# Optimization experiments

Measured on AMD Instinct MI355X. Metric: run time of the kernel, lower is better.

The kernel has to match this reference:

```python
import jax, jax.numpy as jnp
import numpy as np

TOTAL = 262144
NUM_SEG = 1024
H_DIM = 64
BF = 2  # block_flag_num
EPS = 1e-5


def setup_inputs() -> dict:
    key = jax.random.key(0)
    ks = jax.random.split(key, 12)
    # equal-length contiguous segments (ragged in general; equal here for setup)
    bounds = np.arange(0, TOTAL + 1, TOTAL // NUM_SEG, dtype=np.int64)
    seq_start_end = jnp.asarray(np.stack([bounds[:-1], bounds[1:]], axis=1))
    d_in = BF * 2          # 4
    d_emb = BF * 16        # 32
    d_pre = d_emb + H_DIM  # 96
    s = lambda n: 1.0 / np.sqrt(n)
    return {
        'h_state': jax.random.normal(ks[0], (TOTAL, H_DIM), jnp.float32),
        'end_block_pos_rel': jax.random.normal(ks[1], (TOTAL, 2, BF), jnp.float32),
        'W_sp': jax.random.normal(ks[2], (d_emb, d_in), jnp.float32) * s(d_in),
        'b_sp': jnp.zeros((d_emb,), jnp.float32),
        'W1': jax.random.normal(ks[3], (512, d_pre), jnp.float32) * s(d_pre),
        'b1': jnp.zeros((512,), jnp.float32),
        'g1': jnp.ones((512,), jnp.float32),
        'be1': jnp.zeros((512,), jnp.float32),
        'W2': jax.random.normal(ks[4], (1024, 512), jnp.float32) * s(512),
        'b2': jnp.zeros((1024,), jnp.float32),
        'g2': jnp.ones((1024,), jnp.float32),
        'be2': jnp.zeros((1024,), jnp.float32),
        'seq_start_end': seq_start_end,
    }


def _segment_bn(x, seg_ids, counts, gamma, beta):
    # training-mode BatchNorm1d computed independently per segment (biased var)
    num_seg = counts.shape[0]
    mean = jax.ops.segment_sum(x, seg_ids, num_segments=num_seg) / counts[:, None]
    ex2 = jax.ops.segment_sum(x * x, seg_ids, num_segments=num_seg) / counts[:, None]
    var = ex2 - mean * mean
    xn = (x - mean[seg_ids]) * jax.lax.rsqrt(var[seg_ids] + EPS)
    return xn * gamma + beta


def reference(h_state, end_block_pos_rel, W_sp, b_sp, W1, b1, g1, be1, W2, b2, g2, be2, seq_start_end):
    total = h_state.shape[0]
    starts = seq_start_end[:, 0]
    # contiguous segments: segment id of each row
    seg_ids = jnp.searchsorted(starts, jnp.arange(total), side='right') - 1
    counts = (seq_start_end[:, 1] - seq_start_end[:, 0]).astype(h_state.dtype)
    # permute(0,2,1).view(n,-1): (total, 2, BF) -> (total, BF*2)
    pos = jnp.transpose(end_block_pos_rel, (0, 2, 1)).reshape(total, -1)
    rel_emb = pos @ W_sp.T + b_sp                              # (total, 32)
    mlp_in = jnp.concatenate([rel_emb, h_state], axis=1)       # (total, 96)
    h1 = jax.nn.relu(_segment_bn(mlp_in @ W1.T + b1, seg_ids, counts, g1, be1))
    out = jax.nn.relu(_segment_bn(h1 @ W2.T + b2, seg_ids, counts, g2, be2))
    return out  # (total, 1024)
```

## Files before the change

kernel.cpp:

```cpp
#include <hip/hip_runtime.h>
#include <hip/hip_bf16.h>

#define TOTALROWS 262144
#define NSEG      1024
#define SEGROWS   256
#define HD        64
#define DEMB      32
#define DPRE      96
#define N1        512
#define N2        1024
#define EPSB      1e-5f

typedef short s16x8 __attribute__((ext_vector_type(8)));
typedef float f32x4 __attribute__((ext_vector_type(4)));

static __device__ __forceinline__ ushort f2bf(float x) {
    union { float f; unsigned u; } v; v.f = x;
    unsigned r = v.u + 0x7FFFu + ((v.u >> 16) & 1u);
    return (ushort)(r >> 16);
}

static __device__ __forceinline__ void gload_lds16(const void* g, void* l) {
    __builtin_amdgcn_global_load_lds(
        (const __attribute__((address_space(1))) void*)g,
        (__attribute__((address_space(3))) void*)l, 16, 0, 0);
}

__global__ void convert_w2_kernel(const float* __restrict__ w2, ushort* __restrict__ w2b) {
    int i = blockIdx.x * 256 + threadIdx.x;
    float4 v = ((const float4*)w2)[i];
    ushort4 o;
    o.x = f2bf(v.x); o.y = f2bf(v.y); o.z = f2bf(v.z); o.w = f2bf(v.w);
    ((ushort4*)w2b)[i] = o;
}

__global__ __launch_bounds__(512, 2) void layer1_kernel(
    const float* __restrict__ hstate, const float* __restrict__ ebpr,
    const float* __restrict__ Wsp, const float* __restrict__ W1,
    const float* __restrict__ g1, const float* __restrict__ be1,
    ushort* __restrict__ h1)
{
    __shared__ __align__(16) ushort As[SEGROWS * 104];
    __shared__ __align__(16) ushort Bs[SEGROWS * 104];
    __shared__ float statsS[8][4][16];
    __shared__ float statsQ[8][4][16];

    const int seg  = blockIdx.x;
    const int ct   = blockIdx.y;
    const int tid  = threadIdx.x;
    const int lane = tid & 63, wid = tid >> 6;
    const int wr   = wid >> 2, wc = wid & 3;

    {
        const float4* hs4 = (const float4*)(hstate + (size_t)seg * SEGROWS * HD);
        #pragma unroll
        for (int i = 0; i < 8; ++i) {
            int u = tid + i * 512;
            int r = u >> 4, c4 = u & 15;
            float4 v = hs4[u];
            ushort* dst = &As[r * 104 + DEMB + c4 * 4];
            dst[0] = f2bf(v.x); dst[1] = f2bf(v.y); dst[2] = f2bf(v.z); dst[3] = f2bf(v.w);
        }
        #pragma unroll
        for (int i = 0; i < 16; ++i) {
            int u = tid + i * 512;
            int r = u >> 5, k = u & 31;
            float4 e = ((const float4*)ebpr)[seg * SEGROWS + r];
            float4 w = ((const float4*)Wsp)[k];
            float val = w.x * e.x + w.y * e.z + w.z * e.y + w.w * e.w;
            As[r * 104 + k] = f2bf(val);
        }
    }
    {
        const float4* w14 = (const float4*)(W1 + (size_t)ct * 256 * DPRE);
        #pragma unroll
        for (int i = 0; i < 12; ++i) {
            int u = tid + i * 512;
            int r = u / 24, c4 = u % 24;
            float4 v = w14[u];
            ushort* dst = &Bs[r * 104 + c4 * 4];
            dst[0] = f2bf(v.x); dst[1] = f2bf(v.y); dst[2] = f2bf(v.z); dst[3] = f2bf(v.w);
        }
    }
    __syncthreads();

    f32x4 acc[8][4] = {};
    const int arow0 = wr * 128 + (lane & 15);
    const int bcol0 = wc * 64  + (lane & 15);
    const int kg    = (lane >> 4) * 8;
    #pragma unroll
    for (int ks = 0; ks < 3; ++ks) {
        s16x8 af[8], bfr[4];
        #pragma unroll
        for (int m = 0; m < 8; ++m)
            af[m] = *(const s16x8*)&As[(arow0 + m * 16) * 104 + ks * 32 + kg];
        #pragma unroll
        for (int n = 0; n < 4; ++n)
            bfr[n] = *(const s16x8*)&Bs[(bcol0 + n * 16) * 104 + ks * 32 + kg];
        #pragma unroll
        for (int m = 0; m < 8; ++m)
            #pragma unroll
            for (int n = 0; n < 4; ++n)
                acc[m][n] = __builtin_amdgcn_mfma_f32_16x16x32_bf16(af[m], bfr[n], acc[m][n], 0, 0, 0);
    }

    float s[4], q[4];
    #pragma unroll
    for (int n = 0; n < 4; ++n) { s[n] = 0.f; q[n] = 0.f; }
    #pragma unroll
    for (int m = 0; m < 8; ++m)
        #pragma unroll
        for (int n = 0; n < 4; ++n)
            #pragma unroll
            for (int j = 0; j < 4; ++j) { float v = acc[m][n][j]; s[n] += v; q[n] += v * v; }
    #pragma unroll
    for (int n = 0; n < 4; ++n) {
        s[n] += __shfl_xor(s[n], 16); q[n] += __shfl_xor(q[n], 16);
        s[n] += __shfl_xor(s[n], 32); q[n] += __shfl_xor(q[n], 32);
    }
    if ((lane >> 4) == 0) {
        #pragma unroll
        for (int n = 0; n < 4; ++n) { statsS[wid][n][lane] = s[n]; statsQ[wid][n][lane] = q[n]; }
    }
    __syncthreads();

    const float inv256 = 1.0f / 256.0f;
    float aa[4], bb[4];
    const int c16 = lane & 15;
    #pragma unroll
    for (int n = 0; n < 4; ++n) {
        float sum = statsS[wc][n][c16] + statsS[4 + wc][n][c16];
        float sq  = statsQ[wc][n][c16] + statsQ[4 + wc][n][c16];
        float mean = sum * inv256;
        float var  = sq * inv256 - mean * mean;
        float rinv = rsqrtf(var + EPSB);
        int col = ct * 256 + wc * 64 + n * 16 + c16;
        aa[n] = g1[col] * rinv;
        bb[n] = be1[col] - mean * aa[n];
    }

    ushort* outp = h1 + (size_t)(seg * SEGROWS) * N1 + ct * 256;
    const int rbase = wr * 128 + (lane >> 4) * 4;
    #pragma unroll
    for (int m = 0; m < 8; ++m)
        #pragma unroll
        for (int j = 0; j < 4; ++j) {
            int r = rbase + m * 16 + j;
            ushort* rowp = outp + (size_t)r * N1 + wc * 64 + c16;
            #pragma unroll
            for (int n = 0; n < 4; ++n) {
                float v = acc[m][n][j] * aa[n] + bb[n];
                v = v > 0.f ? v : 0.f;
                rowp[n * 16] = f2bf(v);
            }
        }
}


static __device__ __forceinline__ void stage_step(
    const char* gA, const char* gB, ushort* lA, ushort* lB,
    int t, int wid, int lane)
{
    const int rsub = lane >> 2;
    const int cb   = (((lane & 3) ^ ((lane >> 3) & 3)) << 4);
    #pragma unroll
    for (int i = 0; i < 2; ++i) {
        int g = i * 8 + wid;
        size_t go = (size_t)(g * 16 + rsub) * 1024 + (size_t)t * 64 + cb;
        gload_lds16(gA + go, (char*)lA + g * 1024);
        gload_lds16(gB + go, (char*)lB + g * 1024);
    }
}

static __device__ __forceinline__ void compute_step(
    const ushort* lA, const ushort* lB, f32x4 (&acc)[8][4],
    int arow0, int bcol0, int swz)
{
    s16x8 af[8], bfr[4];
    #pragma unroll
    for (int m = 0; m < 8; ++m)
        af[m] = *(const s16x8*)&lA[(arow0 + m * 16) * 32 + swz];
    #pragma unroll
    for (int n = 0; n < 4; ++n)
        bfr[n] = *(const s16x8*)&lB[(bcol0 + n * 16) * 32 + swz];
    __builtin_amdgcn_s_setprio(1);
    #pragma unroll
    for (int m = 0; m < 8; ++m)
        #pragma unroll
        for (int n = 0; n < 4; ++n)
            acc[m][n] = __builtin_amdgcn_mfma_f32_16x16x32_bf16(af[m], bfr[n], acc[m][n], 0, 0, 0);
    __builtin_amdgcn_s_setprio(0);
}

__global__ __launch_bounds__(512, 2) void layer2_kernel(
    const ushort* __restrict__ h1, const ushort* __restrict__ W2b,
    const float* __restrict__ g2, const float* __restrict__ be2,
    float* __restrict__ out)
{
    __shared__ __align__(16) ushort As[4][SEGROWS * 32];
    __shared__ __align__(16) ushort Bs[4][256 * 32];
    __shared__ float statsS[8][4][16];
    __shared__ float statsQ[8][4][16];

    const int b   = blockIdx.x;
    const int wg  = (b & 7) * 512 + (b >> 3);
    const int seg = wg >> 2;
    const int ct  = wg & 3;

    const int tid  = threadIdx.x;
    const int lane = tid & 63, wid = tid >> 6;
    const int wr   = wid >> 2, wc = wid & 3;

    const char* srcA = (const char*)(h1  + (size_t)seg * SEGROWS * N1);
    const char* srcB = (const char*)(W2b + (size_t)ct  * 256    * N1);

    f32x4 acc[8][4] = {};
    const int arow0 = wr * 128 + (lane & 15);
    const int bcol0 = wc * 64  + (lane & 15);
    const int swz  = (((lane >> 4) ^ ((lane >> 1) & 3)) << 3);

    stage_step(srcA, srcB, As[0], Bs[0], 0, wid, lane);
    stage_step(srcA, srcB, As[1], Bs[1], 1, wid, lane);
    stage_step(srcA, srcB, As[2], Bs[2], 2, wid, lane);

#define L2_STEP(T, VW)                                                           \
    {                                                                            \
        if ((T) + 3 < 16)                                                        \
            stage_step(srcA, srcB, As[((T)+3)&3], Bs[((T)+3)&3], (T)+3, wid, lane); \
        asm volatile("s_waitcnt vmcnt(" #VW ")" ::: "memory");                   \
        __builtin_amdgcn_s_barrier();                                            \
        compute_step(As[(T)&3], Bs[(T)&3], acc, arow0, bcol0, swz);              \
        __builtin_amdgcn_s_barrier();                                            \
    }

    L2_STEP(0, 12)  L2_STEP(1, 12)  L2_STEP(2, 12)  L2_STEP(3, 12)
    L2_STEP(4, 12)  L2_STEP(5, 12)  L2_STEP(6, 12)  L2_STEP(7, 12)
    L2_STEP(8, 12)  L2_STEP(9, 12)  L2_STEP(10, 12) L2_STEP(11, 12)
    L2_STEP(12, 12) L2_STEP(13, 8)  L2_STEP(14, 4)  L2_STEP(15, 0)
#undef L2_STEP

    float s[4], q[4];
    #pragma unroll
    for (int n = 0; n < 4; ++n) { s[n] = 0.f; q[n] = 0.f; }
    #pragma unroll
    for (int m = 0; m < 8; ++m)
        #pragma unroll
        for (int n = 0; n < 4; ++n)
            #pragma unroll
            for (int j = 0; j < 4; ++j) { float v = acc[m][n][j]; s[n] += v; q[n] += v * v; }
    #pragma unroll
    for (int n = 0; n < 4; ++n) {
        s[n] += __shfl_xor(s[n], 16); q[n] += __shfl_xor(q[n], 16);
        s[n] += __shfl_xor(s[n], 32); q[n] += __shfl_xor(q[n], 32);
    }
    if ((lane >> 4) == 0) {
        #pragma unroll
        for (int n = 0; n < 4; ++n) { statsS[wid][n][lane] = s[n]; statsQ[wid][n][lane] = q[n]; }
    }
    __syncthreads();

    const float inv256 = 1.0f / 256.0f;
    float aa[4], bb[4];
    const int c16 = lane & 15;
    #pragma unroll
    for (int n = 0; n < 4; ++n) {
        float sum = statsS[wc][n][c16] + statsS[4 + wc][n][c16];
        float sq  = statsQ[wc][n][c16] + statsQ[4 + wc][n][c16];
        float mean = sum * inv256;
        float var  = sq * inv256 - mean * mean;
        float rinv = rsqrtf(var + EPSB);
        int col = ct * 256 + wc * 64 + n * 16 + c16;
        aa[n] = g2[col] * rinv;
        bb[n] = be2[col] - mean * aa[n];
    }

    float* outp = out + (size_t)(seg * SEGROWS) * N2 + ct * 256;
    const int rbase = wr * 128 + (lane >> 4) * 4;
    #pragma unroll
    for (int m = 0; m < 8; ++m)
        #pragma unroll
        for (int j = 0; j < 4; ++j) {
            int r = rbase + m * 16 + j;
            float* rowp = outp + (size_t)r * N2 + wc * 64 + c16;
            #pragma unroll
            for (int n = 0; n < 4; ++n) {
                float v = acc[m][n][j] * aa[n] + bb[n];
                v = v > 0.f ? v : 0.f;
                rowp[n * 16] = v;
            }
        }
}

extern "C" void kernel_launch(void* const* d_in, const int* in_sizes, int n_in,
                              void* d_out, int out_size, void* d_ws, size_t ws_size,
                              hipStream_t stream) {
    const float* hstate = (const float*)d_in[0];
    const float* ebpr   = (const float*)d_in[1];
    const float* Wsp    = (const float*)d_in[2];
    const float* W1     = (const float*)d_in[4];
    const float* g1     = (const float*)d_in[6];
    const float* be1    = (const float*)d_in[7];
    const float* W2     = (const float*)d_in[8];
    const float* g2     = (const float*)d_in[10];
    const float* be2    = (const float*)d_in[11];
    float* outp         = (float*)d_out;

    ushort* h1  = (ushort*)d_ws;
    ushort* W2b = h1 + (size_t)TOTALROWS * N1;

    convert_w2_kernel<<<dim3((N2 * N1 / 4) / 256), dim3(256), 0, stream>>>(W2, W2b);
    layer1_kernel<<<dim3(NSEG, 2), dim3(512), 0, stream>>>(hstate, ebpr, Wsp, W1, g1, be1, h1);
    layer2_kernel<<<dim3(4096), dim3(512), 0, stream>>>(h1, W2b, g2, be2, outp);
}
```

Measured before the change: 634.8 us.

## Restructure layer2 GEMM main loop into four-phase ping-pong with interleaved staging

The layer2 GEMM main loop now uses K tiles of 64 instead of 32, with double-buffered LDS split into row halves and a new XOR swizzle. Each K tile runs as four MFMA quadrant phases, and each phase issues part of the next tile's global-to-LDS loads between the fragment reads and its barrier. The aim is to hide load latency behind MFMA work and to halve the number of loop iterations and barrier pairs. In exchange it adds more barriers per tile, keeps more fragments live in registers, and adds intricate buffer-reuse ordering that could race if the waitcnt and barrier placement is wrong.

```diff
diff --git a/kernel.cpp b/kernel.cpp
--- a/kernel.cpp
+++ b/kernel.cpp
@@ -157,48 +157,64 @@
 }
 
 
-static __device__ __forceinline__ void stage_step(
-    const char* gA, const char* gB, ushort* lA, ushort* lB,
-    int t, int wid, int lane)
-{
-    const int rsub = lane >> 2;
-    const int cb   = (((lane & 3) ^ ((lane >> 3) & 3)) << 4);
-    #pragma unroll
-    for (int i = 0; i < 2; ++i) {
-        int g = i * 8 + wid;
-        size_t go = (size_t)(g * 16 + rsub) * 1024 + (size_t)t * 64 + cb;
-        gload_lds16(gA + go, (char*)lA + g * 1024);
-        gload_lds16(gB + go, (char*)lB + g * 1024);
-    }
-}
-
-static __device__ __forceinline__ void compute_step(
-    const ushort* lA, const ushort* lB, f32x4 (&acc)[8][4],
-    int arow0, int bcol0, int swz)
-{
-    s16x8 af[8], bfr[4];
-    #pragma unroll
-    for (int m = 0; m < 8; ++m)
-        af[m] = *(const s16x8*)&lA[(arow0 + m * 16) * 32 + swz];
-    #pragma unroll
-    for (int n = 0; n < 4; ++n)
-        bfr[n] = *(const s16x8*)&lB[(bcol0 + n * 16) * 32 + swz];
+static __device__ __forceinline__ void stage_half(
+    const char* gsrc, char* ldst, int kt, int wid, int lane)
+{
+    const int row = (wid << 3) + (lane >> 3);
+    const int cl  = (lane & 7) ^ (lane >> 3);
+    const char* g = gsrc + (size_t)row * 1024 + (size_t)kt * 128 + cl * 16;
+    gload_lds16(g,          ldst + wid * 1024);
+    gload_lds16(g + 65536,  ldst + 8192 + wid * 1024);
+}
+
+static __device__ __forceinline__ void read_a4(
+    s16x8 (&dst)[4][2], const ushort* base, int arow0, int mofs, int ko0, int ko1)
+{
+    #pragma unroll
+    for (int mi = 0; mi < 4; ++mi) {
+        const ushort* p = base + (arow0 + (mofs + mi) * 16) * 64;
+        dst[mi][0] = *(const s16x8*)(p + ko0);
+        dst[mi][1] = *(const s16x8*)(p + ko1);
+    }
+}
+static __device__ __forceinline__ void read_b2(
+    s16x8 (&dst)[2][2], const ushort* base, int bcol0, int nofs, int ko0, int ko1)
+{
+    #pragma unroll
+    for (int ni = 0; ni < 2; ++ni) {
+        const ushort* p = base + (bcol0 + (nofs + ni) * 16) * 64;
+        dst[ni][0] = *(const s16x8*)(p + ko0);
+        dst[ni][1] = *(const s16x8*)(p + ko1);
+    }
+}
+static __device__ __forceinline__ void mfma_q(
+    f32x4 (&acc)[8][4], const s16x8 (&af)[4][2], const s16x8 (&bfr)[2][2],
+    int mofs, int nofs)
+{
     __builtin_amdgcn_s_setprio(1);
     #pragma unroll
-    for (int m = 0; m < 8; ++m)
-        #pragma unroll
-        for (int n = 0; n < 4; ++n)
-            acc[m][n] = __builtin_amdgcn_mfma_f32_16x16x32_bf16(af[m], bfr[n], acc[m][n], 0, 0, 0);
+    for (int mi = 0; mi < 4; ++mi)
+        #pragma unroll
+        for (int ni = 0; ni < 2; ++ni) {
+            f32x4 c = acc[mofs + mi][nofs + ni];
+            c = __builtin_amdgcn_mfma_f32_16x16x32_bf16(af[mi][0], bfr[ni][0], c, 0, 0, 0);
+            c = __builtin_amdgcn_mfma_f32_16x16x32_bf16(af[mi][1], bfr[ni][1], c, 0, 0, 0);
+            acc[mofs + mi][nofs + ni] = c;
+        }
     __builtin_amdgcn_s_setprio(0);
 }
+
+#define PHASE_BAR() do { __builtin_amdgcn_sched_barrier(0); \
+    asm volatile("s_barrier" ::: "memory"); \
+    __builtin_amdgcn_sched_barrier(0); } while (0)
 
 __global__ __launch_bounds__(512, 2) void layer2_kernel(
     const ushort* __restrict__ h1, const ushort* __restrict__ W2b,
     const float* __restrict__ g2, const float* __restrict__ be2,
     float* __restrict__ out)
 {
-    __shared__ __align__(16) ushort As[4][SEGROWS * 32];
-    __shared__ __align__(16) ushort Bs[4][256 * 32];
+    __shared__ __align__(16) ushort Asl[2 * 256 * 64];
+    __shared__ __align__(16) ushort Bsl[2 * 256 * 64];
     __shared__ float statsS[8][4][16];
     __shared__ float statsQ[8][4][16];
 
@@ -217,27 +233,52 @@
     f32x4 acc[8][4] = {};
     const int arow0 = wr * 128 + (lane & 15);
     const int bcol0 = wc * 64  + (lane & 15);
-    const int swz  = (((lane >> 4) ^ ((lane >> 1) & 3)) << 3);
-
-    stage_step(srcA, srcB, As[0], Bs[0], 0, wid, lane);
-    stage_step(srcA, srcB, As[1], Bs[1], 1, wid, lane);
-    stage_step(srcA, srcB, As[2], Bs[2], 2, wid, lane);
-
-#define L2_STEP(T, VW)                                                           \
-    {                                                                            \
-        if ((T) + 3 < 16)                                                        \
-            stage_step(srcA, srcB, As[((T)+3)&3], Bs[((T)+3)&3], (T)+3, wid, lane); \
-        asm volatile("s_waitcnt vmcnt(" #VW ")" ::: "memory");                   \
-        __builtin_amdgcn_s_barrier();                                            \
-        compute_step(As[(T)&3], Bs[(T)&3], acc, arow0, bcol0, swz);              \
-        __builtin_amdgcn_s_barrier();                                            \
-    }
-
-    L2_STEP(0, 12)  L2_STEP(1, 12)  L2_STEP(2, 12)  L2_STEP(3, 12)
-    L2_STEP(4, 12)  L2_STEP(5, 12)  L2_STEP(6, 12)  L2_STEP(7, 12)
-    L2_STEP(8, 12)  L2_STEP(9, 12)  L2_STEP(10, 12) L2_STEP(11, 12)
-    L2_STEP(12, 12) L2_STEP(13, 8)  L2_STEP(14, 4)  L2_STEP(15, 0)
-#undef L2_STEP
+    const int ko0 = (((lane >> 4)    ) ^ (lane & 7)) * 8;
+    const int ko1 = (((lane >> 4) + 4) ^ (lane & 7)) * 8;
+
+    stage_half(srcA,          (char*)Asl,          0, wid, lane);
+    stage_half(srcA + 131072, (char*)Asl + 16384,  0, wid, lane);
+    stage_half(srcB,          (char*)Bsl,          0, wid, lane);
+    stage_half(srcB + 131072, (char*)Bsl + 16384,  0, wid, lane);
+    stage_half(srcA,          (char*)Asl + 32768,  1, wid, lane);
+    asm volatile("s_waitcnt vmcnt(2)" ::: "memory");
+    PHASE_BAR();
+
+#define L2_TILE(U, VW)                                                              \
+    {                                                                               \
+        const ushort* Ab = Asl + ((U) & 1) * 16384;                                 \
+        const ushort* Bb = Bsl + ((U) & 1) * 16384;                                 \
+        char* Acur = (char*)Asl + ((U) & 1) * 32768;                                \
+        char* An   = (char*)Asl + (((U) + 1) & 1) * 32768;                          \
+        char* Bn   = (char*)Bsl + (((U) + 1) & 1) * 32768;                          \
+        s16x8 a03[4][2], a47[4][2], b01[2][2], b23[2][2];                           \
+         \
+        read_a4(a03, Ab, arow0, 0, ko0, ko1);                                       \
+        read_b2(b01, Bb, bcol0, 0, ko0, ko1);                                       \
+        if ((U) + 1 < 8) stage_half(srcA + 131072, An + 16384, (U) + 1, wid, lane); \
+        PHASE_BAR();                                                                \
+        mfma_q(acc, a03, b01, 0, 0);                                                \
+                        \
+        read_a4(a47, Ab, arow0, 4, ko0, ko1);                                       \
+        if ((U) + 1 < 8) stage_half(srcB, Bn, (U) + 1, wid, lane);                  \
+        PHASE_BAR();                                                                \
+        mfma_q(acc, a47, b01, 4, 0);                                                \
+                        \
+        read_b2(b23, Bb, bcol0, 2, ko0, ko1);                                       \
+        if ((U) + 1 < 8) stage_half(srcB + 131072, Bn + 16384, (U) + 1, wid, lane); \
+        PHASE_BAR();                                                                \
+        mfma_q(acc, a47, b23, 4, 2);                                                \
+            \
+            \
+        if ((U) + 2 < 8) stage_half(srcA, Acur, (U) + 2, wid, lane);                \
+        asm volatile("s_waitcnt vmcnt(" #VW ")" ::: "memory");                      \
+        PHASE_BAR();                                                                \
+        mfma_q(acc, a03, b23, 0, 2);                                                \
+    }
+
+    L2_TILE(0, 2) L2_TILE(1, 2) L2_TILE(2, 2) L2_TILE(3, 2)
+    L2_TILE(4, 2) L2_TILE(5, 2) L2_TILE(6, 0) L2_TILE(7, 0)
+#undef L2_TILE
 
     float s[4], q[4];
     #pragma unroll
```

Result: faster. 603.7 us (-4.9%).
